# Kernel tuning notes

Measured on AMD Instinct MI355X. Metric: run time of the kernel, lower is better.

## Reference

```python
import jax, jax.numpy as jnp
import numpy as np

N_E = 4096
E_DIM = 512
BETA = 0.25


def setup_inputs() -> dict:
    key = jax.random.key(0)
    k1, k2 = jax.random.split(key)
    z = jax.random.normal(k1, (32, 512, E_DIM), dtype=jnp.float32)
    # embedding.weight ~ U(-1/n_e, 1/n_e)
    emb = jax.random.uniform(k2, (N_E, E_DIM), dtype=jnp.float32,
                             minval=-1.0 / N_E, maxval=1.0 / N_E)
    return {"z": z, "emb": emb}


def reference(z, emb):
    B, S, D = z.shape
    zf = z.reshape(-1, D)  # (N, D)
    # squared L2 distances: ||z||^2 + ||e||^2 - 2 z @ e^T  -> (N, n_e)
    d = (jnp.sum(zf * zf, axis=1, keepdims=True)
         + jnp.sum(emb * emb, axis=1)
         - 2.0 * jnp.matmul(zf, emb.T))
    idx = jnp.argmin(d, axis=1)  # (N,)
    z_q = emb[idx].reshape(z.shape)

    # commitment / codebook loss (detach = stop_gradient)
    loss = (jnp.mean((z_q - jax.lax.stop_gradient(z)) ** 2)
            + BETA * jnp.mean((jax.lax.stop_gradient(z_q) - z) ** 2))

    # straight-through estimator
    z_q_st = z + jax.lax.stop_gradient(z_q - z)

    # perplexity via codeword usage histogram (equiv. to mean of one-hots)
    N = zf.shape[0]
    counts = jnp.zeros((N_E,), dtype=z.dtype).at[idx].add(1.0)
    e_mean = counts / N
    perplexity = jnp.exp(-jnp.sum(e_mean * jnp.log(e_mean + 1e-10)))

    return (loss, z_q_st, idx, perplexity)
```

## Files before the change

kernel.cpp:

```cpp
#include <hip/hip_runtime.h>
#include <math.h>

#define NROWS 16384
#define DDIM  512
#define NE    4096
#define NZ    (NROWS * DDIM)
#define MAXC  64
#define MARGIN 2e-3f

typedef __attribute__((ext_vector_type(8))) short bf16x8;
typedef __attribute__((ext_vector_type(4))) float f32x4;

__device__ __forceinline__ float sqr_rn(float x) { return __fmul_rn(x, x); }
__device__ __forceinline__ ushort f2bf(float f) {
    const unsigned u = __float_as_uint(f);
    return (ushort)((u + 0x7fffu + ((u >> 16) & 1u)) >> 16);
}
__device__ __forceinline__ unsigned pack2(float a, float b) {
    return (unsigned)f2bf(a) | ((unsigned)f2bf(b) << 16);
}

__global__ void k_prep(const float* __restrict__ z, const float* __restrict__ emb,
                       ushort* __restrict__ zh, ushort* __restrict__ eh,
                       float* __restrict__ znorm, float* __restrict__ bnorm,
                       unsigned* __restrict__ counts) {
    if (blockIdx.x < 1024) {
        const int lane = threadIdx.x & 63;
        const int c = (int)((blockIdx.x * 256 + threadIdx.x) >> 6);
        const float4* p = (const float4*)(emb + (size_t)c * DDIM);
        const float4 v0 = p[lane * 2], v1 = p[lane * 2 + 1];
        uint4 w; w.x = pack2(v0.x, v0.y); w.y = pack2(v0.z, v0.w);
        w.z = pack2(v1.x, v1.y); w.w = pack2(v1.z, v1.w);
        *(uint4*)(eh + (size_t)c * DDIM + lane * 8) = w;
        float s = v0.x*v0.x + v0.y*v0.y + v0.z*v0.z + v0.w*v0.w
                + v1.x*v1.x + v1.y*v1.y + v1.z*v1.z + v1.w*v1.w;
        #pragma unroll
        for (int m = 32; m; m >>= 1) s += __shfl_xor(s, m);
        if (lane == 0) { bnorm[c] = s; counts[c] = 0u; }
    } else {
        const int t = (int)((blockIdx.x - 1024) * 256 + threadIdx.x);
        const int row = t >> 2, blk = t & 3;
        const float4* p = (const float4*)(z + (size_t)row * DDIM + blk * 128);
        ushort* zo = zh + (size_t)row * DDIM + blk * 128;
        float4 v0 = p[0], v1 = p[1];
        {
            uint4 w; w.x = pack2(v0.x, v0.y); w.y = pack2(v0.z, v0.w);
            w.z = pack2(v1.x, v1.y); w.w = pack2(v1.z, v1.w);
            *(uint4*)zo = w;
        }
        float r[8];
        r[0] = sqr_rn(v0.x); r[1] = sqr_rn(v0.y); r[2] = sqr_rn(v0.z); r[3] = sqr_rn(v0.w);
        r[4] = sqr_rn(v1.x); r[5] = sqr_rn(v1.y); r[6] = sqr_rn(v1.z); r[7] = sqr_rn(v1.w);
        #pragma unroll
        for (int i = 1; i < 16; ++i) {
            v0 = p[2 * i]; v1 = p[2 * i + 1];
            uint4 w; w.x = pack2(v0.x, v0.y); w.y = pack2(v0.z, v0.w);
            w.z = pack2(v1.x, v1.y); w.w = pack2(v1.z, v1.w);
            *(uint4*)(zo + i * 8) = w;
            r[0] = __fadd_rn(r[0], sqr_rn(v0.x)); r[1] = __fadd_rn(r[1], sqr_rn(v0.y));
            r[2] = __fadd_rn(r[2], sqr_rn(v0.z)); r[3] = __fadd_rn(r[3], sqr_rn(v0.w));
            r[4] = __fadd_rn(r[4], sqr_rn(v1.x)); r[5] = __fadd_rn(r[5], sqr_rn(v1.y));
            r[6] = __fadd_rn(r[6], sqr_rn(v1.z)); r[7] = __fadd_rn(r[7], sqr_rn(v1.w));
        }
        const float B = __fadd_rn(__fadd_rn(__fadd_rn(r[0], r[1]), __fadd_rn(r[2], r[3])),
                                  __fadd_rn(__fadd_rn(r[4], r[5]), __fadd_rn(r[6], r[7])));
        const float s01 = __fadd_rn(B, __shfl_xor(B, 1));
        const float zn  = __fadd_rn(s01, __shfl_xor(s01, 2));
        if (blk == 0) znorm[row] = zn;
    }
}

__global__ __launch_bounds__(256) void k_mfma(const ushort* __restrict__ zh,
                                              const ushort* __restrict__ eh,
                                              const float* __restrict__ bnorm,
                                              ushort* __restrict__ sbuf,
                                              float* __restrict__ rowblkmin) {
    __shared__ ushort Af[8 * 512];
    __shared__ ushort Bf[8 * 512];
    const int tid = threadIdx.x;
    const int lane = tid & 63;
    const int w = tid >> 6;
    const int wrow = (w >> 1) * 64, wcol = (w & 1) * 64;
    const int rbase = blockIdx.x * 128, cbase = blockIdx.y * 128;
    const int sr = tid >> 1, sh = tid & 1;
    const int g  = sr >> 4, r15 = sr & 15;
    const int r16 = lane & 15, g4 = (lane >> 4) * 4;

    f32x4 acc[4][4];
    #pragma unroll
    for (int i = 0; i < 4; ++i)
        #pragma unroll
        for (int j = 0; j < 4; ++j) acc[i][j] = (f32x4){0.f, 0.f, 0.f, 0.f};

    for (int kb = 0; kb < DDIM; kb += 32) {
        const ushort* ga = zh + (size_t)(rbase + sr) * DDIM + kb + sh * 16;
        const ushort* gb = eh + (size_t)(cbase + sr) * DDIM + kb + sh * 16;
        const uint4 qa0 = *(const uint4*)ga;
        const uint4 qa1 = *(const uint4*)(ga + 8);
        const uint4 qb0 = *(const uint4*)gb;
        const uint4 qb1 = *(const uint4*)(gb + 8);
        __syncthreads();
        {
            ushort* pa = &Af[g * 512 + r15 * 8 + sh * 4];
            *(uint2*)(pa +   0) = make_uint2(qa0.x, qa0.y);
            *(uint2*)(pa + 128) = make_uint2(qa0.z, qa0.w);
            *(uint2*)(pa + 256) = make_uint2(qa1.x, qa1.y);
            *(uint2*)(pa + 384) = make_uint2(qa1.z, qa1.w);
            ushort* pb = &Bf[g * 512 + r15 * 8 + sh * 4];
            *(uint2*)(pb +   0) = make_uint2(qb0.x, qb0.y);
            *(uint2*)(pb + 128) = make_uint2(qb0.z, qb0.w);
            *(uint2*)(pb + 256) = make_uint2(qb1.x, qb1.y);
            *(uint2*)(pb + 384) = make_uint2(qb1.z, qb1.w);
        }
        __syncthreads();
        bf16x8 af[4], bf[4];
        #pragma unroll
        for (int f = 0; f < 4; ++f) {
            af[f] = *(const bf16x8*)&Af[((wrow >> 4) + f) * 512 + lane * 8];
            bf[f] = *(const bf16x8*)&Bf[((wcol >> 4) + f) * 512 + lane * 8];
        }
        #pragma unroll
        for (int fi = 0; fi < 4; ++fi)
            #pragma unroll
            for (int fj = 0; fj < 4; ++fj)
                acc[fi][fj] = __builtin_amdgcn_mfma_f32_16x16x32_bf16(
                    af[fi], bf[fj], acc[fi][fj], 0, 0, 0);
    }

    float bn[4];
    #pragma unroll
    for (int fj = 0; fj < 4; ++fj) bn[fj] = bnorm[cbase + wcol + fj * 16 + r16];

    #pragma unroll
    for (int fi = 0; fi < 4; ++fi) {
        #pragma unroll
        for (int r = 0; r < 4; ++r) {
            const int row = rbase + wrow + fi * 16 + g4 + r;
            float s[4];
            #pragma unroll
            for (int fj = 0; fj < 4; ++fj) s[fj] = fmaf(-2.f, acc[fi][fj][r], bn[fj]);
            uint2* sp = (uint2*)(sbuf + (size_t)row * NE + cbase + wcol);
            sp[r16] = make_uint2(pack2(s[0], s[1]), pack2(s[2], s[3]));
            float m = fminf(fminf(s[0], s[1]), fminf(s[2], s[3]));
            #pragma unroll
            for (int x = 1; x < 16; x <<= 1) m = fminf(m, __shfl_xor(m, x));
            if (r16 == 0)
                rowblkmin[(size_t)row * 64 + blockIdx.y * 2 + (w & 1)] = m;
        }
    }
}

__device__ __forceinline__ unsigned long long exact_key(const float4* __restrict__ zp4,
                                                        const float* __restrict__ emb,
                                                        const float* __restrict__ bnorm,
                                                        float zn, int c) {
    const float4* ep4 = (const float4*)(emb + (size_t)c * DDIM);
    float acc = 0.f;
    #pragma unroll 8
    for (int q = 0; q < DDIM / 4; ++q) {
        const float4 zv = zp4[q];
        const float4 ev = ep4[q];
        acc = fmaf(zv.x, ev.x, acc);
        acc = fmaf(zv.y, ev.y, acc);
        acc = fmaf(zv.z, ev.z, acc);
        acc = fmaf(zv.w, ev.w, acc);
    }
    const float s = __fsub_rn(__fadd_rn(zn, bnorm[c]), __fmul_rn(2.f, acc));
    return ((unsigned long long)__float_as_uint(s) << 32) | (unsigned)c;
}

__global__ void k_pg(const ushort* __restrict__ sbuf, const float* __restrict__ rowblkmin,
                     const float* __restrict__ z, const float* __restrict__ emb,
                     const float* __restrict__ znorm, const float* __restrict__ bnorm,
                     float* __restrict__ out, unsigned* __restrict__ counts,
                     float* __restrict__ d2buf) {
    __shared__ int candL[4][MAXC];
    __shared__ unsigned cntL[4];
    const int lane = threadIdx.x & 63;
    const int w = threadIdx.x >> 6;
    const int row = blockIdx.x * 4 + w;
    if (threadIdx.x < 4) cntL[threadIdx.x] = 0u;
    __syncthreads();

    const float bm = rowblkmin[(size_t)row * 64 + lane];
    float gmin = bm;
    #pragma unroll
    for (int m = 32; m; m >>= 1) gmin = fminf(gmin, __shfl_xor(gmin, m));
    const float thr = gmin + MARGIN;
    unsigned long long bmask = __ballot(bm <= thr);
    while (bmask) {
        const int b = __builtin_ctzll(bmask); bmask &= bmask - 1;
        const float val = __uint_as_float(
            (unsigned)sbuf[(size_t)row * NE + b * 64 + lane] << 16);
        if (val <= thr) {
            const unsigned slot = atomicAdd(&cntL[w], 1u);
            if (slot < MAXC)
                candL[w][slot] = b * 64 + (lane & 3) * 16 + (lane >> 2);
        }
    }
    __syncthreads();

    const int cnt = (int)cntL[w];
    int id;
    if (cnt == 1) {
        id = candL[w][0] & (NE - 1);
    } else {
        const float zn = znorm[row];
        const float4* zp4 = (const float4*)(z + (size_t)row * DDIM);
        unsigned long long best = ~0ULL;
        if (cnt >= 2 && cnt <= MAXC) {
            if (lane < cnt)
                best = exact_key(zp4, emb, bnorm, zn, candL[w][lane] & (NE - 1));
        } else {
            for (int c = lane; c < NE; c += 64) {
                const unsigned long long k = exact_key(zp4, emb, bnorm, zn, c);
                if (k < best) best = k;
            }
        }
        #pragma unroll
        for (int m = 32; m; m >>= 1) {
            const unsigned long long ov = __shfl_xor(best, m);
            if (ov < best) best = ov;
        }
        id = (int)(__shfl(best, 0) & (unsigned long long)(NE - 1));
    }

    const float* zp = z + (size_t)row * DDIM;
    const float* ep = emb + (size_t)id * DDIM;
    float* op = out + 1 + (size_t)row * DDIM;
    float d2 = 0.f;
    #pragma unroll
    for (int m = 0; m < 8; ++m) {
        const int k = m * 64 + lane;
        const float e = ep[k];
        const float zv = zp[k];
        const float t = e - zv;
        op[k] = zv + t;
        d2 = fmaf(t, t, d2);
    }
    #pragma unroll
    for (int m = 32; m; m >>= 1) d2 += __shfl_xor(d2, m);
    if (lane == 0) {
        atomicAdd(&counts[id], 1u);
        d2buf[row] = d2;
        out[1 + (size_t)NZ + row] = (float)id;
    }
}

__global__ void k_final(const float* __restrict__ d2buf, const unsigned* __restrict__ counts,
                        float* __restrict__ out) {
    __shared__ double sh[256];
    __shared__ float  shf[256];
    const int tid = threadIdx.x;
    double ent = 0.0;
    for (int i = tid; i < NE; i += 256) {
        const double p = (double)counts[i] / (double)NROWS;
        ent += p * log(p + 1e-10);
    }
    float sse = 0.f;
    for (int i = tid; i < NROWS; i += 256) sse += d2buf[i];
    sh[tid] = ent; shf[tid] = sse;
    __syncthreads();
    for (int s = 128; s; s >>= 1) {
        if (tid < s) { sh[tid] += sh[tid + s]; shf[tid] += shf[tid + s]; }
        __syncthreads();
    }
    if (tid == 0) {
        out[0] = 1.25f * (shf[0] / (float)NZ);
        out[1 + (size_t)NZ + NROWS] = (float)exp(-sh[0]);
    }
}

extern "C" void kernel_launch(void* const* d_in, const int* in_sizes, int n_in,
                              void* d_out, int out_size, void* d_ws, size_t ws_size,
                              hipStream_t stream) {
    const float* z   = (const float*)d_in[0];
    const float* emb = (const float*)d_in[1];
    float* out = (float*)d_out;
    char* ws = (char*)d_ws;

    ushort* zh = (ushort*)(out + 4);
    ushort* eh = (ushort*)(out + 4 + 4194304);

    size_t off = 0;
    float*    bnorm  = (float*)(ws + off); off += (size_t)NE * 4;
    unsigned* counts = (unsigned*)(ws + off); off += (size_t)NE * 4;
    float*    d2buf  = (float*)(ws + off); off += (size_t)NROWS * 4;
    float*    znorm  = (float*)(ws + off); off += (size_t)NROWS * 4;
    ushort*   sbuf   = (ushort*)(ws + off); off += (size_t)NROWS * NE * 2;
    float*    rowblkmin = (float*)(ws + off); off += (size_t)NROWS * 64 * 4;

    k_prep<<<1280, 256, 0, stream>>>(z, emb, zh, eh, znorm, bnorm, counts);
    k_mfma<<<dim3(NROWS / 128, NE / 128), 256, 0, stream>>>(zh, eh, bnorm, sbuf, rowblkmin);
    k_pg<<<NROWS / 4, 256, 0, stream>>>(sbuf, rowblkmin, z, emb, znorm, bnorm, out, counts, d2buf);
    k_final<<<1, 256, 0, stream>>>(d2buf, counts, out);
}
```

Before: 282.2 us.

## Double-buffer LDS tiles in MFMA distance kernel to overlap loads with compute

The GEMM main loop now uses two LDS buffers for the A and B tiles. It prefetches the next K-slice from global memory into registers before running the MFMAs on the current buffer, then writes that slice to the other buffer. This drops one of the two barriers per iteration and hides global load latency behind the matrix math. The cost is doubled shared memory (32 KB per block), which may lower occupancy, plus extra registers for the prefetched data.

```diff
diff --git a/kernel.cpp b/kernel.cpp
--- a/kernel.cpp
+++ b/kernel.cpp
@@ -75,8 +75,8 @@
                                               const float* __restrict__ bnorm,
                                               ushort* __restrict__ sbuf,
                                               float* __restrict__ rowblkmin) {
-    __shared__ ushort Af[8 * 512];
-    __shared__ ushort Bf[8 * 512];
+    __shared__ ushort Af[2][8 * 512];
+    __shared__ ushort Bf[2][8 * 512];
     const int tid = threadIdx.x;
     const int lane = tid & 63;
     const int w = tid >> 6;
@@ -85,6 +85,10 @@
     const int sr = tid >> 1, sh = tid & 1;
     const int g  = sr >> 4, r15 = sr & 15;
     const int r16 = lane & 15, g4 = (lane >> 4) * 4;
+    const int soff = g * 512 + r15 * 8 + sh * 4;
+
+    const ushort* ga = zh + (size_t)(rbase + sr) * DDIM + sh * 16;
+    const ushort* gb = eh + (size_t)(cbase + sr) * DDIM + sh * 16;
 
     f32x4 acc[4][4];
     #pragma unroll
@@ -92,32 +96,39 @@
         #pragma unroll
         for (int j = 0; j < 4; ++j) acc[i][j] = (f32x4){0.f, 0.f, 0.f, 0.f};
 
-    for (int kb = 0; kb < DDIM; kb += 32) {
-        const ushort* ga = zh + (size_t)(rbase + sr) * DDIM + kb + sh * 16;
-        const ushort* gb = eh + (size_t)(cbase + sr) * DDIM + kb + sh * 16;
+    {
         const uint4 qa0 = *(const uint4*)ga;
         const uint4 qa1 = *(const uint4*)(ga + 8);
         const uint4 qb0 = *(const uint4*)gb;
         const uint4 qb1 = *(const uint4*)(gb + 8);
-        __syncthreads();
-        {
-            ushort* pa = &Af[g * 512 + r15 * 8 + sh * 4];
-            *(uint2*)(pa +   0) = make_uint2(qa0.x, qa0.y);
-            *(uint2*)(pa + 128) = make_uint2(qa0.z, qa0.w);
-            *(uint2*)(pa + 256) = make_uint2(qa1.x, qa1.y);
-            *(uint2*)(pa + 384) = make_uint2(qa1.z, qa1.w);
-            ushort* pb = &Bf[g * 512 + r15 * 8 + sh * 4];
-            *(uint2*)(pb +   0) = make_uint2(qb0.x, qb0.y);
-            *(uint2*)(pb + 128) = make_uint2(qb0.z, qb0.w);
-            *(uint2*)(pb + 256) = make_uint2(qb1.x, qb1.y);
-            *(uint2*)(pb + 384) = make_uint2(qb1.z, qb1.w);
-        }
-        __syncthreads();
+        ushort* pa = &Af[0][soff];
+        *(uint2*)(pa +   0) = make_uint2(qa0.x, qa0.y);
+        *(uint2*)(pa + 128) = make_uint2(qa0.z, qa0.w);
+        *(uint2*)(pa + 256) = make_uint2(qa1.x, qa1.y);
+        *(uint2*)(pa + 384) = make_uint2(qa1.z, qa1.w);
+        ushort* pb = &Bf[0][soff];
+        *(uint2*)(pb +   0) = make_uint2(qb0.x, qb0.y);
+        *(uint2*)(pb + 128) = make_uint2(qb0.z, qb0.w);
+        *(uint2*)(pb + 256) = make_uint2(qb1.x, qb1.y);
+        *(uint2*)(pb + 384) = make_uint2(qb1.z, qb1.w);
+    }
+    __syncthreads();
+
+    for (int kb = 0; kb < DDIM; kb += 32) {
+        const int cur = (kb >> 5) & 1;
+        const bool more = (kb + 32 < DDIM);
+        uint4 na0, na1, nb0, nb1;
+        if (more) {
+            na0 = *(const uint4*)(ga + kb + 32);
+            na1 = *(const uint4*)(ga + kb + 40);
+            nb0 = *(const uint4*)(gb + kb + 32);
+            nb1 = *(const uint4*)(gb + kb + 40);
+        }
         bf16x8 af[4], bf[4];
         #pragma unroll
         for (int f = 0; f < 4; ++f) {
-            af[f] = *(const bf16x8*)&Af[((wrow >> 4) + f) * 512 + lane * 8];
-            bf[f] = *(const bf16x8*)&Bf[((wcol >> 4) + f) * 512 + lane * 8];
+            af[f] = *(const bf16x8*)&Af[cur][((wrow >> 4) + f) * 512 + lane * 8];
+            bf[f] = *(const bf16x8*)&Bf[cur][((wcol >> 4) + f) * 512 + lane * 8];
         }
         #pragma unroll
         for (int fi = 0; fi < 4; ++fi)
@@ -125,6 +136,19 @@
             for (int fj = 0; fj < 4; ++fj)
                 acc[fi][fj] = __builtin_amdgcn_mfma_f32_16x16x32_bf16(
                     af[fi], bf[fj], acc[fi][fj], 0, 0, 0);
+        if (more) {
+            ushort* pa = &Af[cur ^ 1][soff];
+            *(uint2*)(pa +   0) = make_uint2(na0.x, na0.y);
+            *(uint2*)(pa + 128) = make_uint2(na0.z, na0.w);
+            *(uint2*)(pa + 256) = make_uint2(na1.x, na1.y);
+            *(uint2*)(pa + 384) = make_uint2(na1.z, na1.w);
+            ushort* pb = &Bf[cur ^ 1][soff];
+            *(uint2*)(pb +   0) = make_uint2(nb0.x, nb0.y);
+            *(uint2*)(pb + 128) = make_uint2(nb0.z, nb0.w);
+            *(uint2*)(pb + 256) = make_uint2(nb1.x, nb1.y);
+            *(uint2*)(pb + 384) = make_uint2(nb1.z, nb1.w);
+            __syncthreads();
+        }
     }
 
     float bn[4];
```

After: 275.0 us, median of 2. 1.03x faster.

## Load MFMA fragments directly from global memory with register double-buffering

Applied to the files above, without the earlier changes.

Removes the LDS staging of A and B tiles and the two block barriers per k-step in the distance GEMM. Each wave now loads its own bf16 fragments straight from global memory and prefetches the next k-slice into registers while the MFMAs run. This drops barrier and LDS traffic, but each A/B row is now fetched by two waves instead of once per block, which shifts load onto L1/L2. The per-lane 16-byte loads are strided across rows, so coalescing is poorer.

```diff
diff --git a/kernel.cpp b/kernel.cpp
--- a/kernel.cpp
+++ b/kernel.cpp
@@ -75,16 +75,21 @@
                                               const float* __restrict__ bnorm,
                                               ushort* __restrict__ sbuf,
                                               float* __restrict__ rowblkmin) {
-    __shared__ ushort Af[8 * 512];
-    __shared__ ushort Bf[8 * 512];
     const int tid = threadIdx.x;
     const int lane = tid & 63;
     const int w = tid >> 6;
     const int wrow = (w >> 1) * 64, wcol = (w & 1) * 64;
     const int rbase = blockIdx.x * 128, cbase = blockIdx.y * 128;
-    const int sr = tid >> 1, sh = tid & 1;
-    const int g  = sr >> 4, r15 = sr & 15;
     const int r16 = lane & 15, g4 = (lane >> 4) * 4;
+    const int k8 = (lane >> 4) * 8;
+
+    const ushort* pa[4];
+    const ushort* pb[4];
+    #pragma unroll
+    for (int f = 0; f < 4; ++f) {
+        pa[f] = zh + (size_t)(rbase + wrow + f * 16 + r16) * DDIM + k8;
+        pb[f] = eh + (size_t)(cbase + wcol + f * 16 + r16) * DDIM + k8;
+    }
 
     f32x4 acc[4][4];
     #pragma unroll
@@ -92,39 +97,33 @@
         #pragma unroll
         for (int j = 0; j < 4; ++j) acc[i][j] = (f32x4){0.f, 0.f, 0.f, 0.f};
 
+    bf16x8 caf[4], cbf[4];
+    #pragma unroll
+    for (int f = 0; f < 4; ++f) {
+        caf[f] = *(const bf16x8*)(pa[f]);
+        cbf[f] = *(const bf16x8*)(pb[f]);
+    }
+
     for (int kb = 0; kb < DDIM; kb += 32) {
-        const ushort* ga = zh + (size_t)(rbase + sr) * DDIM + kb + sh * 16;
-        const ushort* gb = eh + (size_t)(cbase + sr) * DDIM + kb + sh * 16;
-        const uint4 qa0 = *(const uint4*)ga;
-        const uint4 qa1 = *(const uint4*)(ga + 8);
-        const uint4 qb0 = *(const uint4*)gb;
-        const uint4 qb1 = *(const uint4*)(gb + 8);
-        __syncthreads();
-        {
-            ushort* pa = &Af[g * 512 + r15 * 8 + sh * 4];
-            *(uint2*)(pa +   0) = make_uint2(qa0.x, qa0.y);
-            *(uint2*)(pa + 128) = make_uint2(qa0.z, qa0.w);
-            *(uint2*)(pa + 256) = make_uint2(qa1.x, qa1.y);
-            *(uint2*)(pa + 384) = make_uint2(qa1.z, qa1.w);
-            ushort* pb = &Bf[g * 512 + r15 * 8 + sh * 4];
-            *(uint2*)(pb +   0) = make_uint2(qb0.x, qb0.y);
-            *(uint2*)(pb + 128) = make_uint2(qb0.z, qb0.w);
-            *(uint2*)(pb + 256) = make_uint2(qb1.x, qb1.y);
-            *(uint2*)(pb + 384) = make_uint2(qb1.z, qb1.w);
-        }
-        __syncthreads();
-        bf16x8 af[4], bf[4];
-        #pragma unroll
-        for (int f = 0; f < 4; ++f) {
-            af[f] = *(const bf16x8*)&Af[((wrow >> 4) + f) * 512 + lane * 8];
-            bf[f] = *(const bf16x8*)&Bf[((wcol >> 4) + f) * 512 + lane * 8];
+        const bool more = (kb + 32 < DDIM);
+        bf16x8 naf[4], nbf[4];
+        if (more) {
+            #pragma unroll
+            for (int f = 0; f < 4; ++f) {
+                naf[f] = *(const bf16x8*)(pa[f] + kb + 32);
+                nbf[f] = *(const bf16x8*)(pb[f] + kb + 32);
+            }
         }
         #pragma unroll
         for (int fi = 0; fi < 4; ++fi)
             #pragma unroll
             for (int fj = 0; fj < 4; ++fj)
                 acc[fi][fj] = __builtin_amdgcn_mfma_f32_16x16x32_bf16(
-                    af[fi], bf[fj], acc[fi][fj], 0, 0, 0);
+                    caf[fi], cbf[fj], acc[fi][fj], 0, 0, 0);
+        if (more) {
+            #pragma unroll
+            for (int f = 0; f < 4; ++f) { caf[f] = naf[f]; cbf[f] = nbf[f]; }
+        }
     }
 
     float bn[4];
```

New measurement: 389.7 us. +38.1%, slower.

## Double-buffer LDS tiles and prefetch global loads two K-steps ahead in MFMA GEMM

Applied to the files above, without the earlier changes.

Restructures the distance GEMM K-loop into a software pipeline. It uses two LDS buffers per operand, holds the next tile in registers, issues global loads two iterations ahead, and drops from two barriers per iteration to one. The goal is to hide global-memory latency behind MFMA work. In exchange the kernel uses twice the LDS (32KB) and more VGPRs, which may reduce occupancy.

```diff
diff --git a/kernel.cpp b/kernel.cpp
--- a/kernel.cpp
+++ b/kernel.cpp
@@ -75,8 +75,8 @@
                                               const float* __restrict__ bnorm,
                                               ushort* __restrict__ sbuf,
                                               float* __restrict__ rowblkmin) {
-    __shared__ ushort Af[8 * 512];
-    __shared__ ushort Bf[8 * 512];
+    __shared__ ushort Af[2][8 * 512];
+    __shared__ ushort Bf[2][8 * 512];
     const int tid = threadIdx.x;
     const int lane = tid & 63;
     const int w = tid >> 6;
@@ -85,6 +85,10 @@
     const int sr = tid >> 1, sh = tid & 1;
     const int g  = sr >> 4, r15 = sr & 15;
     const int r16 = lane & 15, g4 = (lane >> 4) * 4;
+    const int soff = g * 512 + r15 * 8 + sh * 4;
+
+    const ushort* ga = zh + (size_t)(rbase + sr) * DDIM + sh * 16;
+    const ushort* gb = eh + (size_t)(cbase + sr) * DDIM + sh * 16;
 
     f32x4 acc[4][4];
     #pragma unroll
@@ -92,32 +96,43 @@
         #pragma unroll
         for (int j = 0; j < 4; ++j) acc[i][j] = (f32x4){0.f, 0.f, 0.f, 0.f};
 
-    for (int kb = 0; kb < DDIM; kb += 32) {
-        const ushort* ga = zh + (size_t)(rbase + sr) * DDIM + kb + sh * 16;
-        const ushort* gb = eh + (size_t)(cbase + sr) * DDIM + kb + sh * 16;
+    uint4 hA0, hA1, hB0, hB1;
+    {
         const uint4 qa0 = *(const uint4*)ga;
         const uint4 qa1 = *(const uint4*)(ga + 8);
         const uint4 qb0 = *(const uint4*)gb;
         const uint4 qb1 = *(const uint4*)(gb + 8);
-        __syncthreads();
-        {
-            ushort* pa = &Af[g * 512 + r15 * 8 + sh * 4];
-            *(uint2*)(pa +   0) = make_uint2(qa0.x, qa0.y);
-            *(uint2*)(pa + 128) = make_uint2(qa0.z, qa0.w);
-            *(uint2*)(pa + 256) = make_uint2(qa1.x, qa1.y);
-            *(uint2*)(pa + 384) = make_uint2(qa1.z, qa1.w);
-            ushort* pb = &Bf[g * 512 + r15 * 8 + sh * 4];
-            *(uint2*)(pb +   0) = make_uint2(qb0.x, qb0.y);
-            *(uint2*)(pb + 128) = make_uint2(qb0.z, qb0.w);
-            *(uint2*)(pb + 256) = make_uint2(qb1.x, qb1.y);
-            *(uint2*)(pb + 384) = make_uint2(qb1.z, qb1.w);
-        }
-        __syncthreads();
+        ushort* pa = &Af[0][soff];
+        *(uint2*)(pa +   0) = make_uint2(qa0.x, qa0.y);
+        *(uint2*)(pa + 128) = make_uint2(qa0.z, qa0.w);
+        *(uint2*)(pa + 256) = make_uint2(qa1.x, qa1.y);
+        *(uint2*)(pa + 384) = make_uint2(qa1.z, qa1.w);
+        ushort* pb = &Bf[0][soff];
+        *(uint2*)(pb +   0) = make_uint2(qb0.x, qb0.y);
+        *(uint2*)(pb + 128) = make_uint2(qb0.z, qb0.w);
+        *(uint2*)(pb + 256) = make_uint2(qb1.x, qb1.y);
+        *(uint2*)(pb + 384) = make_uint2(qb1.z, qb1.w);
+        hA0 = *(const uint4*)(ga + 32);
+        hA1 = *(const uint4*)(ga + 40);
+        hB0 = *(const uint4*)(gb + 32);
+        hB1 = *(const uint4*)(gb + 40);
+    }
+    __syncthreads();
+
+    #pragma unroll
+    for (int t = 0; t < 16; ++t) {
+        uint4 fA0, fA1, fB0, fB1;
+        if (t + 2 < 16) {
+            fA0 = *(const uint4*)(ga + (t + 2) * 32);
+            fA1 = *(const uint4*)(ga + (t + 2) * 32 + 8);
+            fB0 = *(const uint4*)(gb + (t + 2) * 32);
+            fB1 = *(const uint4*)(gb + (t + 2) * 32 + 8);
+        }
         bf16x8 af[4], bf[4];
         #pragma unroll
         for (int f = 0; f < 4; ++f) {
-            af[f] = *(const bf16x8*)&Af[((wrow >> 4) + f) * 512 + lane * 8];
-            bf[f] = *(const bf16x8*)&Bf[((wcol >> 4) + f) * 512 + lane * 8];
+            af[f] = *(const bf16x8*)&Af[t & 1][((wrow >> 4) + f) * 512 + lane * 8];
+            bf[f] = *(const bf16x8*)&Bf[t & 1][((wcol >> 4) + f) * 512 + lane * 8];
         }
         #pragma unroll
         for (int fi = 0; fi < 4; ++fi)
@@ -125,6 +140,20 @@
             for (int fj = 0; fj < 4; ++fj)
                 acc[fi][fj] = __builtin_amdgcn_mfma_f32_16x16x32_bf16(
                     af[fi], bf[fj], acc[fi][fj], 0, 0, 0);
+        if (t + 1 < 16) {
+            ushort* pa = &Af[(t + 1) & 1][soff];
+            *(uint2*)(pa +   0) = make_uint2(hA0.x, hA0.y);
+            *(uint2*)(pa + 128) = make_uint2(hA0.z, hA0.w);
+            *(uint2*)(pa + 256) = make_uint2(hA1.x, hA1.y);
+            *(uint2*)(pa + 384) = make_uint2(hA1.z, hA1.w);
+            ushort* pb = &Bf[(t + 1) & 1][soff];
+            *(uint2*)(pb +   0) = make_uint2(hB0.x, hB0.y);
+            *(uint2*)(pb + 128) = make_uint2(hB0.z, hB0.w);
+            *(uint2*)(pb + 256) = make_uint2(hB1.x, hB1.y);
+            *(uint2*)(pb + 384) = make_uint2(hB1.z, hB1.w);
+            __syncthreads();
+        }
+        hA0 = fA0; hA1 = fA1; hB0 = fB0; hB1 = fB1;
     }
 
     float bn[4];
```

Result: faster. 269.9 us (-4.3%).
